# Kernel optimization log

Measured on AMD Instinct MI355X. Metric: run time of the kernel, lower is better.

The kernel has to match this reference:

```python
import jax, jax.numpy as jnp
import numpy as np

B, C, H, W = 16, 256, 64, 64   # batch, latent_dim, spatial
K = 1024                        # num_codebook_vectors
BETA = 0.25


def setup_inputs() -> dict:
    key = jax.random.key(0)
    k1, k2 = jax.random.split(key)
    z = jax.random.normal(k1, (B, C, H, W), dtype=jnp.float32)
    # torch init: uniform(-1/K, 1/K)
    codebook = jax.random.uniform(k2, (K, C), dtype=jnp.float32,
                                  minval=-1.0 / K, maxval=1.0 / K)
    return {"z": z, "codebook": codebook}


def reference(z, codebook):
    # NCHW -> NHWC, flatten spatial
    zc = jnp.transpose(z, (0, 2, 3, 1))          # [B,H,W,C]
    zf = zc.reshape(-1, zc.shape[-1])            # [N,C]
    # squared euclidean distances to each code: [N,K]
    d = (jnp.sum(zf * zf, axis=1, keepdims=True)
         + jnp.sum(codebook * codebook, axis=1)
         - 2.0 * jnp.matmul(zf, codebook.T))
    idx = jnp.argmin(d, axis=1)                  # [N]
    zq = codebook[idx].reshape(zc.shape)         # [B,H,W,C]
    # commitment / codebook loss (sign convention as in source)
    loss = (jnp.mean((zq - jax.lax.stop_gradient(zc)) ** 2)
            - BETA * jnp.mean((zc - jax.lax.stop_gradient(zq)) ** 2))
    # straight-through estimator
    zq_st = zc + jax.lax.stop_gradient(zq - zc)
    return jnp.transpose(zq_st, (0, 3, 1, 2)), idx, loss
```

## Files before the change

### kernel.cpp

```cpp
#include <hip/hip_runtime.h>
#include <hip/hip_fp16.h>

#define B_    16
#define C_    256
#define HW_   4096
#define CHW_  1048576
#define N_    65536
#define K_    1024
#define FLT_BIG 3.402823466e38f
#define GAP_T  1.2e-4f

typedef _Float16 half8 __attribute__((ext_vector_type(8)));
typedef float   float16 __attribute__((ext_vector_type(16)));

__device__ __forceinline__ unsigned umin_(unsigned a, unsigned b) { return a < b ? a : b; }
__device__ __forceinline__ unsigned umax_(unsigned a, unsigned b) { return a > b ? a : b; }

__global__ void szp_kernel(const float* __restrict__ z, float* __restrict__ rp) {
#pragma clang fp contract(off)
    int hj = blockIdx.x >> 8;
    int bx = blockIdx.x & 255;
    int n  = bx * 256 + threadIdx.x;
    int h = hj >> 3, j = hj & 7;
    const float* p = z + (size_t)(n >> 12) * CHW_ + (n & 4095)
                       + (size_t)(h * 128 + j) * HW_;
    float v = p[0];
    float r = v * v;
    for (int s = 1; s < 16; s++) {
        float u = p[(size_t)(s * 8) * HW_];
        r += u * u;
    }
    rp[(size_t)hj * N_ + n] = r;
}

__global__ void szc_kernel(const float* __restrict__ rp, float* __restrict__ sz) {
#pragma clang fp contract(off)
    int n = blockIdx.x * 256 + threadIdx.x;
    float blk[2];
    for (int h = 0; h < 2; h++) {
        const float* b = rp + (size_t)(h * 8) * N_ + n;
        float r0 = b[0 * N_], r1 = b[1 * N_], r2 = b[2 * N_], r3 = b[3 * N_];
        float r4 = b[4 * N_], r5 = b[5 * N_], r6 = b[6 * N_], r7 = b[7 * N_];
        blk[h] = ((r0 + r1) + (r2 + r3)) + ((r4 + r5) + (r6 + r7));
    }
    sz[n] = blk[0] + blk[1];
}

__global__ void sc_kernel(const float* __restrict__ cb, float* __restrict__ sc) {
#pragma clang fp contract(off)
    int k = blockIdx.x * 256 + threadIdx.x;
    const float* p0 = cb + (size_t)k * C_;
    float blk[2];
    for (int h = 0; h < 2; h++) {
        const float* p = p0 + h * 128;
        float r[8];
#pragma unroll
        for (int j = 0; j < 8; j++) { float v = p[j]; r[j] = v * v; }
        for (int i = 8; i < 128; i += 8) {
#pragma unroll
            for (int j = 0; j < 8; j++) { float v = p[i + j]; r[j] += v * v; }
        }
        blk[h] = ((r[0] + r[1]) + (r[2] + r[3])) + ((r[4] + r[5]) + (r[6] + r[7]));
    }
    sc[k] = blk[0] + blk[1];
}

__global__ void cbh_prep(const float* __restrict__ cb, unsigned short* __restrict__ cbh) {
    int k = blockIdx.x, c = threadIdx.x;
    float v = cb[(size_t)k * C_ + c] * 1024.0f;
    __half hv = __float2half_rn(v);
    size_t F = ((size_t)(c >> 4) * 1024 + k) * 16 + ((c >> 3) & 1) * 8 + (c & 7);
    cbh[F] = __half_as_ushort(hv);
}

__global__ void cbT_prep(const float* __restrict__ cb, float* __restrict__ cbT) {
    int c = blockIdx.x, k = threadIdx.x;
    cbT[(size_t)c * K_ + k] = cb[(size_t)k * C_ + c];
}

__global__ __launch_bounds__(256, 4)
void score_kernel(const float* __restrict__ z, const unsigned short* __restrict__ cbh,
                  const float* __restrict__ sc,
                  float* __restrict__ s1o, float* __restrict__ s2o,
                  int* __restrict__ i1o) {
    __shared__ __align__(16) int zw[64 * 132];
    __shared__ float scs[1024];
    __shared__ float ex[4 * 64 * 4];

    int t = threadIdx.x;
    int w = t >> 6, l = t & 63;
    int n0 = blockIdx.x * 64;

    for (int i = t; i < 1024; i += 256) scs[i] = sc[i] + 0.25f;

    {
        int px = l;
        const float* zp = z + (size_t)(n0 >> 12) * CHW_ + (n0 & 4095) + px;
        int key = (px >> 3) & 3;
#pragma unroll 4
        for (int i = 0; i < 32; i++) {
            int widx = w * 32 + i;
            int c0 = widx * 2;
            float v0 = zp[(size_t)c0 * HW_];
            float v1 = zp[(size_t)(c0 + 1) * HW_];
            unsigned pk = (unsigned)__half_as_ushort(__float2half_rn(v0))
                        | ((unsigned)__half_as_ushort(__float2half_rn(v1)) << 16);
            int c16 = widx >> 2, rem = widx & 3;
            zw[px * 132 + (((c16 ^ key) << 2) | rem)] = pk;
        }
    }
    __syncthreads();

    unsigned b1[2] = { 0xFFFFFFFFu, 0xFFFFFFFFu };
    unsigned b2[2] = { 0xFFFFFFFFu, 0xFFFFFFFFu };

    const unsigned short* ab = cbh + ((size_t)(w * 64 + (l & 31)) * 16 + (l >> 5) * 8);
    short rowmap = (short)((l >> 5) << 2);
    half8 pf[2][2];
#pragma unroll
    for (int i = 0; i < 2; i++) {
        const unsigned short* s = ab + (i & 15) * 16384 + (i >> 4) * 4096;
        pf[i][0] = *(const half8*)(s);
        pf[i][1] = *(const half8*)(s + 512);
    }

    int bkey = ((l & 31) >> 3) & 3;
    int prow0 = (l & 31) * 132;

    for (int chunk = 0; chunk < 4; chunk++) {
        float16 acc[2][2];
#pragma unroll
        for (int mt = 0; mt < 2; mt++)
#pragma unroll
            for (int nt = 0; nt < 2; nt++)
#pragma unroll
                for (int r = 0; r < 16; r++) acc[mt][nt][r] = 0.f;

#pragma unroll
        for (int kk = 0; kk < 16; kk++) {
            int step = chunk * 16 + kk;
            int buf = step & 1;
            half8 a0 = pf[buf][0], a1 = pf[buf][1];
            int ns = step + 2; if (ns > 63) ns = 63;
            {
                const unsigned short* s = ab + (ns & 15) * 16384 + (ns >> 4) * 4096;
                pf[buf][0] = *(const half8*)(s);
                pf[buf][1] = *(const half8*)(s + 512);
            }
            half8 bz[2];
#pragma unroll
            for (int nt = 0; nt < 2; nt++) {
                int c16 = kk * 2 + (l >> 5);
                int word = (nt * 32 * 132 + prow0) + ((c16 ^ bkey) << 2);
                bz[nt] = *(const half8*)((const char*)zw + (size_t)word * 4);
            }
            acc[0][0] = __builtin_amdgcn_mfma_f32_32x32x16_f16(a0, bz[0], acc[0][0], 0, 0, 0);
            acc[0][1] = __builtin_amdgcn_mfma_f32_32x32x16_f16(a0, bz[1], acc[0][1], 0, 0, 0);
            acc[1][0] = __builtin_amdgcn_mfma_f32_32x32x16_f16(a1, bz[0], acc[1][0], 0, 0, 0);
            acc[1][1] = __builtin_amdgcn_mfma_f32_32x32x16_f16(a1, bz[1], acc[1][1], 0, 0, 0);
        }

#pragma unroll
        for (int mt = 0; mt < 2; mt++)
#pragma unroll
            for (int r = 0; r < 16; r++) {
                int scode = chunk * 256 + w * 64 + mt * 32
                          + (r & 3) + ((r >> 2) << 3) + rowmap;
                float sv = scs[scode];
                unsigned emb = (unsigned)((chunk << 5) | (mt << 4) | r);
#pragma unroll
                for (int nt = 0; nt < 2; nt++) {
                    float s = fmaf(-0.001953125f, acc[mt][nt][r], sv);
                    unsigned key = (__float_as_uint(s) & 0xFFFFFF80u) | emb;
                    b2[nt] = umin_(b2[nt], umax_(b1[nt], key));
                    b1[nt] = umin_(b1[nt], key);
                }
            }
    }

#pragma unroll
    for (int nt = 0; nt < 2; nt++) {
        unsigned e1 = b1[nt] & 127u;
        float f1 = __uint_as_float(b1[nt] & 0xFFFFFF80u);
        float f2 = __uint_as_float(b2[nt] & 0xFFFFFF80u);
        int idx = (int)(e1 >> 5) * 256 + w * 64 + (int)((e1 >> 4) & 1) * 32
                + (int)(e1 & 3) + (int)(((e1 >> 2) & 3) << 3) + (int)rowmap;

        float of1 = __shfl_xor(f1, 32, 64);
        int   oi  = __shfl_xor(idx, 32, 64);
        float of2 = __shfl_xor(f2, 32, 64);
        if (of1 < f1 || (of1 == f1 && oi < idx)) {
            f2 = fminf(f1, of2); f1 = of1; idx = oi;
        } else {
            f2 = fminf(f2, of1);
        }

        if (l < 32) {
            int e = (w * 64 + nt * 32 + l) * 4;
            ex[e + 0] = f1;
            ex[e + 1] = f2;
            ((int*)ex)[e + 2] = idx;
        }
    }
    __syncthreads();
    if (t < 64) {
        float cb1 = FLT_BIG, cb2 = FLT_BIG; int cj1 = 0;
#pragma unroll
        for (int wv = 0; wv < 4; wv++) {
            int e = (wv * 64 + t) * 4;
            float nb1 = ex[e + 0];
            float nb2 = ex[e + 1];
            int   nj1 = ((int*)ex)[e + 2];
            if (nb1 < cb1 || (nb1 == cb1 && nj1 < cj1)) {
                cb2 = fminf(cb1, nb2); cb1 = nb1; cj1 = nj1;
            } else {
                cb2 = fminf(cb2, nb1);
            }
        }
        int n = n0 + t;
        s1o[n] = cb1; s2o[n] = cb2; i1o[n] = cj1;
    }
}

__global__ void flag_kernel(const float* __restrict__ s1, const float* __restrict__ s2,
                            const int* __restrict__ i1,
                            int* __restrict__ fidx, float* __restrict__ out_idx,
                            int* __restrict__ list, int* __restrict__ count) {
    int n = blockIdx.x * 256 + threadIdx.x;
    int j = i1[n];
    fidx[n] = j;
    out_idx[n] = (float)j;
    if (s2[n] - s1[n] < GAP_T) {
        int pos = atomicAdd(count, 1);
        list[pos] = n;
    }
}

__global__ void refine_kernel(const float* __restrict__ z, const float* __restrict__ cbT,
                              const float* __restrict__ sz, const float* __restrict__ sc,
                              const int* __restrict__ list, const int* __restrict__ count,
                              int* __restrict__ fidx, float* __restrict__ out_idx) {
    __shared__ double zd[4][256];
    int w = threadIdx.x >> 6, l = threadIdx.x & 63;
    int cnt = *count;
    if (cnt > 65536) cnt = 65536;
    for (int ii = blockIdx.x * 4 + w; ii < cnt; ii += 8192) {
        int n = list[ii];
        const float* zp = z + (size_t)(n >> 12) * CHW_ + (n & 4095);
#pragma unroll
        for (int j = 0; j < 4; j++)
            zd[w][l * 4 + j] = (double)zp[(size_t)(l * 4 + j) * HW_];
        asm volatile("s_waitcnt lgkmcnt(0)" ::: "memory");
        double acc[16];
#pragma unroll
        for (int a = 0; a < 16; a++) acc[a] = 0.0;
        for (int c = 0; c < 256; c++) {
            double zc = zd[w][c];
            const float* cp = cbT + (size_t)c * K_ + l * 4;
#pragma unroll
            for (int it = 0; it < 4; it++) {
                float4 cv = *(const float4*)(cp + it * 256);
                acc[it * 4 + 0] += zc * (double)cv.x;
                acc[it * 4 + 1] += zc * (double)cv.y;
                acc[it * 4 + 2] += zc * (double)cv.z;
                acc[it * 4 + 3] += zc * (double)cv.w;
            }
        }
        float szv = sz[n];
        float best = FLT_BIG; int bidx = K_;
#pragma unroll
        for (int it = 0; it < 4; it++)
#pragma unroll
            for (int s = 0; s < 4; s++) {
                int k = it * 256 + l * 4 + s;
                float dotf = (float)acc[it * 4 + s];
                float dq = (szv + sc[k]) - 2.0f * dotf;
                if (dq < best || (dq == best && k < bidx)) { best = dq; bidx = k; }
            }
#pragma unroll
        for (int off = 32; off > 0; off >>= 1) {
            float ob = __shfl_xor(best, off, 64);
            int   oj = __shfl_xor(bidx, off, 64);
            if (ob < best || (ob == best && oj < bidx)) { best = ob; bidx = oj; }
        }
        if (l == 0) { fidx[n] = bidx; out_idx[n] = (float)bidx; }
        asm volatile("s_waitcnt lgkmcnt(0)" ::: "memory");
    }
}

__global__ void output_kernel(const float* __restrict__ z, const float* __restrict__ cb,
                              const int* __restrict__ fidx,
                              float* __restrict__ out0, double* __restrict__ partials) {
    __shared__ double red[256];
    int t = threadIdx.x;
    int blk = blockIdx.x;
    int n0 = blk * 64;
    int batch = n0 >> 12, s0 = n0 & 4095;
    const float* zbase = z + (size_t)batch * CHW_ + s0;
    float* obase = out0 + (size_t)batch * CHW_ + s0;
    double sum = 0.0;
#pragma unroll 4
    for (int r = 0; r < 64; r++) {
        int f = r * 256 + t;
        int c = f >> 6, i = f & 63;
        int idx = fidx[n0 + i];
        float q  = cb[(size_t)idx * C_ + c];
        float zv = zbase[(size_t)c * HW_ + i];
        obase[(size_t)c * HW_ + i] = q;
        float d = q - zv;
        sum += (double)d * (double)d;
    }
    red[t] = sum;
    __syncthreads();
    for (int s = 128; s > 0; s >>= 1) {
        if (t < s) red[t] += red[t + s];
        __syncthreads();
    }
    if (t == 0) partials[blk] = red[0];
}

__global__ void loss_kernel(const double* __restrict__ partials, float* __restrict__ out_loss) {
    __shared__ double red[256];
    int t = threadIdx.x;
    double s = 0.0;
    for (int r = t; r < 1024; r += 256) s += partials[r];
    red[t] = s;
    __syncthreads();
    for (int k = 128; k > 0; k >>= 1) {
        if (t < k) red[t] += red[t + k];
        __syncthreads();
    }
    if (t == 0) *out_loss = (float)(0.75 * red[0] / 16777216.0);
}

extern "C" void kernel_launch(void* const* d_in, const int* in_sizes, int n_in,
                              void* d_out, int out_size, void* d_ws, size_t ws_size,
                              hipStream_t stream) {
    const float* z  = (const float*)d_in[0];
    const float* cb = (const float*)d_in[1];

    float* out0     = (float*)d_out;
    float* out_idx  = out0 + (size_t)16777216;
    float* out_loss = out0 + (size_t)16842752;

    char* w = (char*)d_ws;
    double* partials = (double*)w;
    float*  sc   = (float*)(w + 8192);
    float*  sz   = (float*)(w + 12288);
    float*  s1   = (float*)(w + 274432);
    float*  s2   = (float*)(w + 536576);
    int*    i1   = (int*)  (w + 798720);
    int*    fidx = (int*)  (w + 1060864);
    int*    count= (int*)  (w + 1323008);
    int*    list = (int*)  (w + 1323264);
    unsigned short* cbh = (unsigned short*)(w + 1585408);
    float*  cbT  = (float*)(w + 2109952);
    float*  rp   = (float*)(w + 3158528);

    hipMemsetAsync(count, 0, 4, stream);
    szp_kernel   <<<4096, 256, 0, stream>>>(z, rp);
    szc_kernel   <<<256,  256, 0, stream>>>(rp, sz);
    sc_kernel    <<<4,    256, 0, stream>>>(cb, sc);
    cbh_prep     <<<1024, 256, 0, stream>>>(cb, cbh);
    cbT_prep     <<<256, 1024, 0, stream>>>(cb, cbT);
    score_kernel <<<1024, 256, 0, stream>>>(z, cbh, sc, s1, s2, i1);
    flag_kernel  <<<256,  256, 0, stream>>>(s1, s2, i1, fidx, out_idx, list, count);
    refine_kernel<<<2048, 256, 0, stream>>>(z, cbT, sz, sc, list, count, fidx, out_idx);
    output_kernel<<<1024, 256, 0, stream>>>(z, cb, fidx, out0, partials);
    loss_kernel  <<<1,    256, 0, stream>>>(partials, out_loss);
}
```

Baseline: 317.0 us.

## Vectorize output gather with 4x4 register transpose and raise MFMA wave priority

The output kernel now stages the 64 block indices in shared memory. Each thread loads four codebook rows as float4 and transposes a 4x4 tile in registers, so z reads and output writes become float4 accesses instead of scalar strided ones. This targets load/store instruction count and the poor coalescing of the per-element codebook gather. The distance kernel also raises wave priority around the MFMA block, to favour issuing matrix instructions over other waves' memory ops.

```diff
diff --git a/kernel.cpp b/kernel.cpp
--- a/kernel.cpp
+++ b/kernel.cpp
@@ -154,10 +154,12 @@
                 int word = (nt * 32 * 132 + prow0) + ((c16 ^ bkey) << 2);
                 bz[nt] = *(const half8*)((const char*)zw + (size_t)word * 4);
             }
+            __builtin_amdgcn_s_setprio(1);
             acc[0][0] = __builtin_amdgcn_mfma_f32_32x32x16_f16(a0, bz[0], acc[0][0], 0, 0, 0);
             acc[0][1] = __builtin_amdgcn_mfma_f32_32x32x16_f16(a0, bz[1], acc[0][1], 0, 0, 0);
             acc[1][0] = __builtin_amdgcn_mfma_f32_32x32x16_f16(a1, bz[0], acc[1][0], 0, 0, 0);
             acc[1][1] = __builtin_amdgcn_mfma_f32_32x32x16_f16(a1, bz[1], acc[1][1], 0, 0, 0);
+            __builtin_amdgcn_s_setprio(0);
         }
 
 #pragma unroll
@@ -291,24 +293,48 @@
 __global__ void output_kernel(const float* __restrict__ z, const float* __restrict__ cb,
                               const int* __restrict__ fidx,
                               float* __restrict__ out0, double* __restrict__ partials) {
+    __shared__ int sidx[64];
     __shared__ double red[256];
     int t = threadIdx.x;
     int blk = blockIdx.x;
     int n0 = blk * 64;
+    if (t < 64) sidx[t] = fidx[n0 + t];
+    __syncthreads();
     int batch = n0 >> 12, s0 = n0 & 4095;
     const float* zbase = z + (size_t)batch * CHW_ + s0;
     float* obase = out0 + (size_t)batch * CHW_ + s0;
+    int ig = (t & 15) * 4;
+    int cg = (t >> 4) * 4;
+    const float* r0 = cb + (size_t)sidx[ig + 0] * C_;
+    const float* r1 = cb + (size_t)sidx[ig + 1] * C_;
+    const float* r2 = cb + (size_t)sidx[ig + 2] * C_;
+    const float* r3 = cb + (size_t)sidx[ig + 3] * C_;
     double sum = 0.0;
-#pragma unroll 4
-    for (int r = 0; r < 64; r++) {
-        int f = r * 256 + t;
-        int c = f >> 6, i = f & 63;
-        int idx = fidx[n0 + i];
-        float q  = cb[(size_t)idx * C_ + c];
-        float zv = zbase[(size_t)c * HW_ + i];
-        obase[(size_t)c * HW_ + i] = q;
-        float d = q - zv;
-        sum += (double)d * (double)d;
+#pragma unroll
+    for (int pass = 0; pass < 4; pass++) {
+        int c0 = pass * 64 + cg;
+        float4 q0 = *(const float4*)(r0 + c0);
+        float4 q1 = *(const float4*)(r1 + c0);
+        float4 q2 = *(const float4*)(r2 + c0);
+        float4 q3 = *(const float4*)(r3 + c0);
+        float a0[4] = { q0.x, q0.y, q0.z, q0.w };
+        float a1[4] = { q1.x, q1.y, q1.z, q1.w };
+        float a2[4] = { q2.x, q2.y, q2.z, q2.w };
+        float a3[4] = { q3.x, q3.y, q3.z, q3.w };
+#pragma unroll
+        for (int j = 0; j < 4; j++) {
+            size_t off = (size_t)(c0 + j) * HW_ + ig;
+            float4 zv = *(const float4*)(zbase + off);
+            float4 qq;
+            qq.x = a0[j]; qq.y = a1[j]; qq.z = a2[j]; qq.w = a3[j];
+            *(float4*)(obase + off) = qq;
+            float d0 = qq.x - zv.x, d1 = qq.y - zv.y;
+            float d2 = qq.z - zv.z, d3 = qq.w - zv.w;
+            sum += (double)d0 * (double)d0;
+            sum += (double)d1 * (double)d1;
+            sum += (double)d2 * (double)d2;
+            sum += (double)d3 * (double)d3;
+        }
     }
     red[t] = sum;
     __syncthreads();
```

Result: faster. 280.1 us (-11.6%).
